# Optimization experiments

Hardware: AMD Instinct MI355X
Metric: run time of the kernel (lower is better)

Reference implementation:

```python
import jax, jax.numpy as jnp
import numpy as np

B, C, H, W = 8, 256, 32, 32
Nh, DK, DV = 8, 64, 64


def conv1x1(x, Wm, b):
    # x: [B,C,H,W], Wm: [O,C] -> [B,O,H,W]
    return jnp.einsum('bchw,oc->bohw', x, Wm) + b[None, :, None, None]


def rel_to_abs(x):
    # x: [B', Nh', L, 2L-1] -> [B', Nh', L, L]
    b, nh, L, _ = x.shape
    x = jnp.pad(x, ((0, 0), (0, 0), (0, 0), (0, 1)))          # [b,nh,L,2L]
    flat = x.reshape(b, nh, L * 2 * L)
    flat = jnp.pad(flat, ((0, 0), (0, 0), (0, L - 1)))
    final = flat.reshape(b, nh, L + 1, 2 * L - 1)
    return final[:, :, :L, L - 1:]


def relative_logits_1d(q, rel_k, Hd, Wd, case):
    # q: [B,Nh,Hd,Wd,dk], rel_k: [2*Wd-1, dk]
    rel = jnp.einsum('bhxyd,md->bhxym', q, rel_k)             # [B,Nh,Hd,Wd,2Wd-1]
    rel = rel.reshape(-1, Nh * Hd, Wd, 2 * Wd - 1)
    rel = rel_to_abs(rel)                                      # [B,Nh*Hd,Wd,Wd]
    rel = rel.reshape(-1, Nh, Hd, Wd, Wd)
    rel = jnp.broadcast_to(rel[:, :, :, None],
                           (rel.shape[0], Nh, Hd, Hd, Wd, Wd))
    if case == 'w':
        rel = rel.transpose((0, 1, 2, 4, 3, 5))                # [B,Nh,H,W,H,W]
    else:  # 'h'
        rel = rel.transpose((0, 1, 4, 2, 5, 3))                # [B,Nh,H,W,H,W]
    return rel.reshape(-1, Nh, Hd * Wd, Hd * Wd)


def setup_inputs() -> dict:
    key = jax.random.key(0)
    ks = jax.random.split(key, 13)
    s = 0.05
    return {
        'q_x': jax.random.normal(ks[0], (B, C, H, W), jnp.float32),
        'k_x': jax.random.normal(ks[1], (B, C, H, W), jnp.float32),
        'v_x': jax.random.normal(ks[2], (B, C, H, W), jnp.float32),
        'Wq': jax.random.normal(ks[3], (Nh * DK, C), jnp.float32) * s,
        'bq': jax.random.normal(ks[4], (Nh * DK,), jnp.float32) * s,
        'Wk': jax.random.normal(ks[5], (Nh * DK, C), jnp.float32) * s,
        'bk': jax.random.normal(ks[6], (Nh * DK,), jnp.float32) * s,
        'Wv': jax.random.normal(ks[7], (Nh * DV, C), jnp.float32) * s,
        'bv': jax.random.normal(ks[8], (Nh * DV,), jnp.float32) * s,
        'Wo': jax.random.normal(ks[9], (DV, Nh * DV), jnp.float32) * s,
        'bo': jax.random.normal(ks[10], (DV,), jnp.float32) * s,
        'key_rel_w': jax.random.normal(ks[11], (2 * W - 1, DK), jnp.float32),
        'key_rel_h': jax.random.normal(ks[12], (2 * H - 1, DK), jnp.float32),
    }


def reference(q_x, k_x, v_x, Wq, bq, Wk, bk, Wv, bv, Wo, bo, key_rel_w, key_rel_h):
    q = conv1x1(q_x, Wq, bq).reshape(B, Nh, DK, H, W) * (DK ** -0.5)
    k = conv1x1(k_x, Wk, bk).reshape(B, Nh, DK, H, W)
    v = conv1x1(v_x, Wv, bv).reshape(B, Nh, DV, H, W)
    flat_q = q.reshape(B, Nh, DK, H * W)
    flat_k = k.reshape(B, Nh, DK, H * W)
    flat_v = v.reshape(B, Nh, DV, H * W)
    # content logits: [B,Nh,HW,HW]
    logits = jnp.einsum('bhdi,bhdj->bhij', flat_q, flat_k)
    # relative logits (Bello et al.)
    qt = q.transpose((0, 1, 3, 4, 2))                          # [B,Nh,H,W,dk]
    w_rel = relative_logits_1d(qt, key_rel_w, H, W, 'w')
    h_rel = relative_logits_1d(qt.transpose((0, 1, 3, 2, 4)), key_rel_h, W, H, 'h')
    logits = logits + h_rel + w_rel
    weights = jax.nn.softmax(logits, axis=-1)
    # [B,Nh,HW,dv] then reshape (NOT transpose) exactly as the torch code does
    attn = jnp.einsum('bhij,bhdj->bhid', weights, flat_v)
    attn = attn.reshape(B, Nh, DV, H, W)
    attn = attn.reshape(B, Nh * DV, H, W)                      # combine heads
    return conv1x1(attn, Wo, bo)                               # [B,dv,H,W]
```

## Files before the change

kernel.cpp:

```cpp
#include <hip/hip_runtime.h>

using f32x4  = __attribute__((ext_vector_type(4))) float;
using f32x16 = __attribute__((ext_vector_type(16))) float;
using bf16x8 = __attribute__((ext_vector_type(8))) short;

__device__ __forceinline__ ushort f2bf(float f) {
  union { float f; unsigned u; } v{f};
  unsigned r = v.u + 0x7FFFu + ((v.u >> 16) & 1u);
  return (ushort)(r >> 16);
}
__device__ __forceinline__ ushort4 f4bf(float4 f) {
  ushort4 r; r.x = f2bf(f.x); r.y = f2bf(f.y); r.z = f2bf(f.z); r.w = f2bf(f.w); return r;
}
__device__ __forceinline__ f32x4 mfma16(bf16x8 a, bf16x8 b, f32x4 c) {
  return __builtin_amdgcn_mfma_f32_16x16x32_bf16(a, b, c, 0, 0, 0);
}
__device__ __forceinline__ f32x16 mfma32(bf16x8 a, bf16x8 b, f32x16 c) {
  return __builtin_amdgcn_mfma_f32_32x32x16_bf16(a, b, c, 0, 0, 0);
}
__device__ __forceinline__ void gload16(const ushort* g, ushort* l) {
  __builtin_amdgcn_global_load_lds(
      (const __attribute__((address_space(1))) void*)g,
      (__attribute__((address_space(3))) void*)l, 16, 0, 0);
}

__global__ __launch_bounds__(256) void prep_all(
    const float* __restrict__ x0, const float* __restrict__ x1,
    const float* __restrict__ x2,
    const float* __restrict__ Wq, const float* __restrict__ Wk,
    const float* __restrict__ Wv, const float* __restrict__ Wo,
    ushort* __restrict__ xT, ushort* __restrict__ Wdst)
{
  __shared__ ushort sT[64 * 72];
  const int bi = blockIdx.x;
  const int t = threadIdx.x;
  if (bi < 1536) {
    const int hw0 = (bi & 15) * 64;
    const int rest = bi >> 4;
    const int y = rest % 12, b = rest / 12;
    const int inp = y >> 2, c0 = (y & 3) * 64;
    const float* src = (inp == 0 ? x0 : inp == 1 ? x1 : x2) +
                       ((size_t)b * 256 + c0) * 1024 + hw0;
    const int clb = t >> 4, hwl = (t & 15) * 4;
#pragma unroll
    for (int cc = 0; cc < 4; ++cc) {
      const int cl = clb + cc * 16;
      const float4 v = *reinterpret_cast<const float4*>(&src[(size_t)cl * 1024 + hwl]);
      *reinterpret_cast<ushort4*>(&sT[cl * 72 + hwl]) = f4bf(v);
    }
    __syncthreads();
    const int hv = t >> 2, cs = (t & 3) * 16;
    ushort tmp[16];
#pragma unroll
    for (int j = 0; j < 16; ++j) tmp[j] = sT[(cs + j) * 72 + hv];
    ushort* dst = xT + (size_t)inp * 2097152 +
                  ((size_t)b * 1024 + hw0 + hv) * 256 + c0 + cs;
    *reinterpret_cast<uint4*>(&dst[0]) = *reinterpret_cast<uint4*>(&tmp[0]);
    *reinterpret_cast<uint4*>(&dst[8]) = *reinterpret_cast<uint4*>(&tmp[8]);
  } else {
    const int idx = ((bi - 1536) * 256 + t) * 8;
    const int r = idx >> 17;
    const float* src = (r == 0 ? Wq : r == 1 ? Wk : r == 2 ? Wv : Wo) + (idx - r * 131072);
    const float4 a = *reinterpret_cast<const float4*>(&src[0]);
    const float4 b = *reinterpret_cast<const float4*>(&src[4]);
    ushort tmp[8];
    *reinterpret_cast<ushort4*>(&tmp[0]) = f4bf(a);
    *reinterpret_cast<ushort4*>(&tmp[4]) = f4bf(b);
    *reinterpret_cast<uint4*>(&Wdst[idx]) = *reinterpret_cast<uint4*>(&tmp[0]);
  }
}

__global__ __launch_bounds__(256) void conv_qkv(
    const ushort* __restrict__ xT, const ushort* __restrict__ WsBf,
    const float* __restrict__ bq, const float* __restrict__ bk,
    const float* __restrict__ bv,
    ushort* __restrict__ outQ, ushort* __restrict__ outK,
    ushort* __restrict__ outV)
{
  __shared__ ushort lds[18432];
  const int z = blockIdx.z, inp = z >> 3, b = z & 7;
  const int t = threadIdx.x, w = t >> 6, lane = t & 63;
  const int li = lane & 15, g = lane >> 4;
  const int o0 = blockIdx.y * 256, hw0 = blockIdx.x * 64;
  const ushort* xb = xT + (size_t)inp * 2097152 + ((size_t)b * 1024 + hw0) * 256;
  const ushort* wb = WsBf + (size_t)inp * 131072 + (size_t)o0 * 256;
  const float* bias = (inp == 0 ? bq : inp == 1 ? bk : bv);
  ushort* out = (inp == 0 ? outQ : inp == 1 ? outK : outV);
  const float scale = (inp == 0) ? 0.125f * 1.44269504f : 1.0f;
  const int MODE = (inp == 2);
  const int srow = t >> 2, sseg = t & 3;

  f32x4 acc[4][4];
#pragma unroll
  for (int i = 0; i < 4; ++i)
#pragma unroll
    for (int j = 0; j < 4; ++j) acc[i][j] = f32x4{0.f, 0.f, 0.f, 0.f};

  for (int ks = 0; ks < 8; ++ks) {
    const int k0 = ks * 32;
    __syncthreads();
    *reinterpret_cast<uint4*>(&lds[srow * 40 + sseg * 8]) =
        *reinterpret_cast<const uint4*>(&xb[(size_t)srow * 256 + k0 + sseg * 8]);
#pragma unroll
    for (int it = 0; it < 4; ++it) {
      const int r = srow + it * 64;
      *reinterpret_cast<uint4*>(&lds[(64 + r) * 40 + sseg * 8]) =
          *reinterpret_cast<const uint4*>(&wb[(size_t)r * 256 + k0 + sseg * 8]);
    }
    __syncthreads();
    bf16x8 af[4], bf[4];
#pragma unroll
    for (int mi = 0; mi < 4; ++mi) {
      const int ra = (!MODE) ? (mi * 16 + li) : (64 + w * 64 + mi * 16 + li);
      af[mi] = *reinterpret_cast<const bf16x8*>(&lds[ra * 40 + g * 8]);
    }
#pragma unroll
    for (int ni = 0; ni < 4; ++ni) {
      const int rb = (!MODE) ? (64 + w * 64 + ni * 16 + li) : (ni * 16 + li);
      bf[ni] = *reinterpret_cast<const bf16x8*>(&lds[rb * 40 + g * 8]);
    }
#pragma unroll
    for (int mi = 0; mi < 4; ++mi)
#pragma unroll
      for (int ni = 0; ni < 4; ++ni)
        acc[mi][ni] = mfma16(af[mi], bf[ni], acc[mi][ni]);
  }
  __syncthreads();

  if (!MODE) {
    float bb[4];
#pragma unroll
    for (int ni = 0; ni < 4; ++ni) bb[ni] = bias[o0 + w * 64 + ni * 16 + li];
#pragma unroll
    for (int mi = 0; mi < 4; ++mi)
#pragma unroll
      for (int ni = 0; ni < 4; ++ni)
#pragma unroll
        for (int r = 0; r < 4; ++r)
          lds[(mi * 16 + g * 4 + r) * 264 + w * 64 + ni * 16 + li] =
              f2bf((acc[mi][ni][r] + bb[ni]) * scale);
    __syncthreads();
    const int row = t & 63;
    ushort* dst = out + (size_t)(b * 8 + (o0 >> 6) + w) * 65536 +
                  (size_t)(hw0 + row) * 64;
#pragma unroll
    for (int seg = 0; seg < 8; ++seg)
      *reinterpret_cast<uint4*>(&dst[seg * 8]) =
          *reinterpret_cast<const uint4*>(&lds[row * 264 + w * 64 + seg * 8]);
  } else {
    const int lis = (li & 3) | ((li & 4) << 1) | ((li & 8) >> 1);
#pragma unroll
    for (int mi = 0; mi < 4; ++mi)
#pragma unroll
      for (int r = 0; r < 4; ++r) {
        const float bb = bias[o0 + w * 64 + mi * 16 + g * 4 + r];
#pragma unroll
        for (int ni = 0; ni < 4; ++ni)
          lds[w * 4608 + (mi * 16 + g * 4 + r) * 72 + ni * 16 + lis] =
              f2bf(acc[mi][ni][r] + bb);
      }
    __syncthreads();
    const int d = t & 63;
    ushort* dst = out + (size_t)(b * 8 + (o0 >> 6) + w) * 65536 +
                  (size_t)d * 1024 + hw0;
#pragma unroll
    for (int seg = 0; seg < 8; ++seg)
      *reinterpret_cast<uint4*>(&dst[seg * 8]) =
          *reinterpret_cast<const uint4*>(&lds[w * 4608 + d * 72 + seg * 8]);
  }
}

__global__ __launch_bounds__(256) void outconv_mfma(
    const float* __restrict__ attnF, const ushort* __restrict__ Wob,
    const float* __restrict__ bias, float* __restrict__ out)
{
  __shared__ float ldsf[64 * 68];
  ushort* lds = reinterpret_cast<ushort*>(ldsf);
  const int t = threadIdx.x, w = t >> 6, lane = t & 63;
  const int li = lane & 15, g = lane >> 4;
  const int b = blockIdx.y, hw0 = blockIdx.x * 64;
  f32x4 acc[4];
#pragma unroll
  for (int i = 0; i < 4; ++i) acc[i] = f32x4{0.f, 0.f, 0.f, 0.f};

  for (int ks = 0; ks < 16; ++ks) {
    const int k0 = ks * 32;
    __syncthreads();
    *reinterpret_cast<uint4*>(&lds[(t >> 2) * 40 + (t & 3) * 8]) =
        *reinterpret_cast<const uint4*>(&Wob[(size_t)(t >> 2) * 512 + k0 + (t & 3) * 8]);
#pragma unroll
    for (int it = 0; it < 2; ++it) {
      const int c = (t >> 4) + it * 16;
      const float4 v = *reinterpret_cast<const float4*>(
          &attnF[((size_t)b * 512 + k0 + c) * 1024 + hw0 + (t & 15) * 4]);
      const int swz = c ^ ((t & 3) << 3);
      const float vv[4] = {v.x, v.y, v.z, v.w};
#pragma unroll
      for (int j = 0; j < 4; ++j)
        lds[2560 + ((t & 15) * 4 + j) * 40 + swz] = f2bf(vv[j]);
    }
    __syncthreads();
    const bf16x8 bfg = *reinterpret_cast<const bf16x8*>(
        &lds[2560 + (w * 16 + li) * 40 + 8 * (g ^ ((li >> 2) & 3))]);
#pragma unroll
    for (int mi = 0; mi < 4; ++mi) {
      const bf16x8 af = *reinterpret_cast<const bf16x8*>(&lds[(mi * 16 + li) * 40 + g * 8]);
      acc[mi] = mfma16(af, bfg, acc[mi]);
    }
  }
  __syncthreads();
#pragma unroll
  for (int mi = 0; mi < 4; ++mi)
#pragma unroll
    for (int r = 0; r < 4; ++r)
      ldsf[(mi * 16 + g * 4 + r) * 68 + w * 16 + li] =
          acc[mi][r] + bias[mi * 16 + g * 4 + r];
  __syncthreads();
  const int o = t >> 2, cs = (t & 3) * 16;
  float* dst = out + ((size_t)b * 64 + o) * 1024 + hw0;
#pragma unroll
  for (int f = 0; f < 4; ++f)
    *reinterpret_cast<float4*>(&dst[cs + f * 4]) =
        *reinterpret_cast<const float4*>(&ldsf[o * 68 + cs + f * 4]);
}

__global__ __launch_bounds__(256, 3) void attn_mfma(
    const ushort* __restrict__ qg, const ushort* __restrict__ kg,
    const ushort* __restrict__ vg, const float* __restrict__ relw,
    const float* __restrict__ relh, float* __restrict__ attn)
{
  __shared__ __align__(16) unsigned char smem[50176];
  ushort* kv0 = (ushort*)smem;
  ushort* kv1 = (ushort*)(smem + 16384);
  float*  scratch = (float*)(smem + 16384);
  float*  rhc = (float*)(smem + 32768);

  const int bid = blockIdx.x;
  const int bn = bid & 63;
  const int qb = (bid >> 6) * 128;
  const int tid = threadIdx.x;
  const int w = tid >> 6, lane = tid & 63;
  const int li32 = lane & 31, h = lane >> 5;
  const int so = lane & 7;

  const ushort* qbn = qg + (size_t)bn * 65536;
  const ushort* kbn = kg + (size_t)bn * 65536;
  const ushort* vbn = vg + (size_t)bn * 65536;

  const int ldr = lane >> 3;
  auto stage = [&](int cc) {
    ushort* dst = (cc & 1) ? kv1 : kv0;
    if (w < 2) {
#pragma unroll
      for (int inst = 0; inst < 4; ++inst) {
        const int row = w * 32 + inst * 8 + ldr;
        const int col8 = ((lane & 7) ^ (row & 7)) * 8;
        gload16(&kbn[(cc * 64 + row) * 64 + col8],
                &dst[(w * 32 + inst * 8) * 64]);
      }
    } else {
#pragma unroll
      for (int inst = 0; inst < 4; ++inst) {
        const int dv = (w - 2) * 32 + inst * 8 + ldr;
        const int col8 = ((lane & 7) ^ (dv & 7)) * 8;
        gload16(&vbn[dv * 1024 + cc * 64 + col8],
                &dst[4096 + ((w - 2) * 32 + inst * 8) * 64]);
      }
    }
  };

  stage(0);

  const int qi = qb + w * 32 + li32;
  bf16x8 qf[4];
#pragma unroll
  for (int ks = 0; ks < 4; ++ks)
    qf[ks] = *reinterpret_cast<const bf16x8*>(&qbn[qi * 64 + ks * 16 + 8 * h]);

  const int xq = (qb + w * 32) >> 5;

  float* tbw = scratch + (size_t)(w * 32) * 66;
  float rwv[16];
#pragma unroll
  for (int mt = 0; mt < 2; ++mt) {
    f32x16 d;
#pragma unroll
    for (int e = 0; e < 16; ++e) d[e] = 0.f;
    const int mm = min(mt * 32 + li32, 62);
#pragma unroll
    for (int ks = 0; ks < 4; ++ks) {
      float tmp[8];
      *reinterpret_cast<float4*>(&tmp[0]) =
          *reinterpret_cast<const float4*>(&relw[mm * 64 + ks * 16 + 8 * h]);
      *reinterpret_cast<float4*>(&tmp[4]) =
          *reinterpret_cast<const float4*>(&relw[mm * 64 + ks * 16 + 8 * h + 4]);
      bf16x8 af;
#pragma unroll
      for (int e = 0; e < 8; ++e) af[e] = (short)f2bf(tmp[e]);
      d = mfma32(af, qf[ks], d);
    }
#pragma unroll
    for (int r = 0; r < 16; ++r)
      tbw[li32 * 66 + mt * 32 + ((r & 3) + 8 * (r >> 2) + 4 * h)] = d[r];
  }
  asm volatile("s_waitcnt lgkmcnt(0)" ::: "memory");
  __builtin_amdgcn_sched_barrier(0);
#pragma unroll
  for (int r = 0; r < 16; ++r)
    rwv[r] = tbw[li32 * 65 + ((r & 3) + 8 * (r >> 2) + 4 * h) + 31];
  asm volatile("s_waitcnt lgkmcnt(0)" ::: "memory");
  __builtin_amdgcn_sched_barrier(0);
  __syncthreads();

#pragma unroll
  for (int mt = 0; mt < 2; ++mt) {
    f32x16 d;
#pragma unroll
    for (int e = 0; e < 16; ++e) d[e] = 0.f;
    const int mm = min(mt * 32 + li32, 62);
#pragma unroll
    for (int ks = 0; ks < 4; ++ks) {
      float tmp[8];
      *reinterpret_cast<float4*>(&tmp[0]) =
          *reinterpret_cast<const float4*>(&relh[mm * 64 + ks * 16 + 8 * h]);
      *reinterpret_cast<float4*>(&tmp[4]) =
          *reinterpret_cast<const float4*>(&relh[mm * 64 + ks * 16 + 8 * h + 4]);
      bf16x8 af;
#pragma unroll
      for (int e = 0; e < 8; ++e) af[e] = (short)f2bf(tmp[e]);
      d = mfma32(af, qf[ks], d);
    }
#pragma unroll
    for (int r = 0; r < 16; ++r) {
      const int m = mt * 32 + ((r & 3) + 8 * (r >> 2) + 4 * h);
      const int idx = m - 31 + xq;
      if ((unsigned)idx < 32u)
        rhc[(w * 32 + li32) * 34 + idx] = d[r];
    }
  }
  asm volatile("s_waitcnt lgkmcnt(0)" ::: "memory");
  __builtin_amdgcn_sched_barrier(0);

  f32x16 oacc0, oacc1;
#pragma unroll
  for (int e = 0; e < 16; ++e) { oacc0[e] = 0.f; oacc1[e] = 0.f; }
  float lrun = 0.f;

  for (int c = 0; c < 16; ++c) {
    __syncthreads();
    if (c < 15) stage(c + 1);
    const ushort* Kb = (c & 1) ? kv1 : kv0;
    const ushort* Vb = Kb + 4096;

    const float2 rhv = *reinterpret_cast<const float2*>(
        &rhc[(w * 32 + li32) * 34 + 2 * c]);
    f32x16 s0, s1;
#pragma unroll
    for (int r = 0; r < 16; ++r) { s0[r] = rwv[r] + rhv.x; s1[r] = rwv[r] + rhv.y; }
    __builtin_amdgcn_s_setprio(1);
#pragma unroll
    for (int ks = 0; ks < 4; ++ks) {
      const int oct = ((2 * ks + h) ^ so) * 8;
      const bf16x8 k0 = *reinterpret_cast<const bf16x8*>(&Kb[li32 * 64 + oct]);
      const bf16x8 k1 = *reinterpret_cast<const bf16x8*>(&Kb[(32 + li32) * 64 + oct]);
      s0 = mfma32(k0, qf[ks], s0);
      s1 = mfma32(k1, qf[ks], s1);
    }
    __builtin_amdgcn_s_setprio(0);

    float psum = 0.f;
#pragma unroll
    for (int r = 0; r < 16; ++r) {
      s0[r] = exp2f(s0[r]);
      s1[r] = exp2f(s1[r]);
      psum += s0[r] + s1[r];
    }
    lrun += psum;

    uint pk0[4][2], pk1[4][2];
#pragma unroll
    for (int J = 0; J < 4; ++J) {
      asm("v_cvt_pk_bf16_f32 %0, %1, %2" : "=v"(pk0[J][0]) : "v"(s0[4 * J]), "v"(s0[4 * J + 1]));
      asm("v_cvt_pk_bf16_f32 %0, %1, %2" : "=v"(pk0[J][1]) : "v"(s0[4 * J + 2]), "v"(s0[4 * J + 3]));
      asm("v_cvt_pk_bf16_f32 %0, %1, %2" : "=v"(pk1[J][0]) : "v"(s1[4 * J]), "v"(s1[4 * J + 1]));
      asm("v_cvt_pk_bf16_f32 %0, %1, %2" : "=v"(pk1[J][1]) : "v"(s1[4 * J + 2]), "v"(s1[4 * J + 3]));
    }

    __builtin_amdgcn_s_setprio(1);
#pragma unroll
    for (int ks = 0; ks < 4; ++ks) {
      const int kk = ks & 1;
      uint fu[4];
      if (ks < 2) {
        fu[0] = pk0[2 * kk][0]; fu[1] = pk0[2 * kk][1];
        fu[2] = pk0[2 * kk + 1][0]; fu[3] = pk0[2 * kk + 1][1];
      } else {
        fu[0] = pk1[2 * kk][0]; fu[1] = pk1[2 * kk][1];
        fu[2] = pk1[2 * kk + 1][0]; fu[3] = pk1[2 * kk + 1][1];
      }
      const bf16x8 pa = *reinterpret_cast<const bf16x8*>(&fu[0]);
      const int oct = ((2 * ks + h) ^ so) * 8;
      const bf16x8 v0 = *reinterpret_cast<const bf16x8*>(&Vb[li32 * 64 + oct]);
      const bf16x8 v1 = *reinterpret_cast<const bf16x8*>(&Vb[(32 + li32) * 64 + oct]);
      oacc0 = mfma32(pa, v0, oacc0);
      oacc1 = mfma32(pa, v1, oacc1);
    }
    __builtin_amdgcn_s_setprio(0);
  }

  const float lt = lrun + __shfl_xor(lrun, 32);
  float* ob = attn + (size_t)bn * 65536;
#pragma unroll
  for (int r = 0; r < 16; ++r) {
    const int rp = (r & 3) + 8 * (r >> 2) + 4 * h;
    const float linv = 1.0f / __shfl(lt, rp);
    const size_t qrow = (size_t)(qb + w * 32 + rp) * 64;
    ob[qrow + li32] = oacc0[r] * linv;
    ob[qrow + 32 + li32] = oacc1[r] * linv;
  }
}

extern "C" void kernel_launch(void* const* d_in, const int* in_sizes, int n_in,
                              void* d_out, int out_size, void* d_ws, size_t ws_size,
                              hipStream_t stream) {
  const float* q_x = (const float*)d_in[0];
  const float* k_x = (const float*)d_in[1];
  const float* v_x = (const float*)d_in[2];
  const float* Wq  = (const float*)d_in[3];
  const float* bq  = (const float*)d_in[4];
  const float* Wk  = (const float*)d_in[5];
  const float* bk  = (const float*)d_in[6];
  const float* Wv  = (const float*)d_in[7];
  const float* bv  = (const float*)d_in[8];
  const float* Wo  = (const float*)d_in[9];
  const float* bo  = (const float*)d_in[10];
  const float* krw = (const float*)d_in[11];
  const float* krh = (const float*)d_in[12];

  ushort* wsQ  = (ushort*)d_ws;
  ushort* wsK  = wsQ + 4194304;
  ushort* wsV  = wsK + 4194304;
  ushort* xT   = wsV + 4194304;
  ushort* WsBf = xT + 6291456;
  float*  attnF = (float*)(WsBf + 425984);

  prep_all<<<1744, 256, 0, stream>>>(q_x, k_x, v_x, Wq, Wk, Wv, Wo, xT, WsBf);

  conv_qkv<<<dim3(16, 2, 24), 256, 0, stream>>>(xT, WsBf, bq, bk, bv, wsQ, wsK, wsV);

  attn_mfma<<<512, 256, 0, stream>>>(wsQ, wsK, wsV, krw, krh, attnF);

  outconv_mfma<<<dim3(16, 8), 256, 0, stream>>>(attnF, WsBf + 393216, bo, (float*)d_out);
}
```

Measured before the change: 90.08 us.

## Halve outconv tile to double block count, use raw exp2 and split sum chains

```diff
diff --git a/kernel.cpp b/kernel.cpp
--- a/kernel.cpp
+++ b/kernel.cpp
@@ -170,15 +170,15 @@
   }
 }
 
-__global__ __launch_bounds__(256) void outconv_mfma(
+__global__ __launch_bounds__(128) void outconv_mfma(
     const float* __restrict__ attnF, const ushort* __restrict__ Wob,
     const float* __restrict__ bias, float* __restrict__ out)
 {
-  __shared__ float ldsf[64 * 68];
-  ushort* lds = reinterpret_cast<ushort*>(ldsf);
-  const int t = threadIdx.x, w = t >> 6, lane = t & 63;
+  __shared__ float ldsf[64 * 36];
+  __shared__ ushort lds[64 * 40 + 32 * 40];
+  const int t = threadIdx.x, wv = t >> 6, lane = t & 63;
   const int li = lane & 15, g = lane >> 4;
-  const int b = blockIdx.y, hw0 = blockIdx.x * 64;
+  const int b = blockIdx.y, hw0 = blockIdx.x * 32;
   f32x4 acc[4];
 #pragma unroll
   for (int i = 0; i < 4; ++i) acc[i] = f32x4{0.f, 0.f, 0.f, 0.f};
@@ -186,22 +186,29 @@
   for (int ks = 0; ks < 16; ++ks) {
     const int k0 = ks * 32;
     __syncthreads();
-    *reinterpret_cast<uint4*>(&lds[(t >> 2) * 40 + (t & 3) * 8]) =
-        *reinterpret_cast<const uint4*>(&Wob[(size_t)(t >> 2) * 512 + k0 + (t & 3) * 8]);
-#pragma unroll
-    for (int it = 0; it < 2; ++it) {
-      const int c = (t >> 4) + it * 16;
-      const float4 v = *reinterpret_cast<const float4*>(
-          &attnF[((size_t)b * 512 + k0 + c) * 1024 + hw0 + (t & 15) * 4]);
-      const int swz = c ^ ((t & 3) << 3);
-      const float vv[4] = {v.x, v.y, v.z, v.w};
-#pragma unroll
-      for (int j = 0; j < 4; ++j)
-        lds[2560 + ((t & 15) * 4 + j) * 40 + swz] = f2bf(vv[j]);
+    {
+      const int row = t & 63, sh = (t >> 6) * 16;
+      *reinterpret_cast<uint4*>(&lds[row * 40 + sh]) =
+          *reinterpret_cast<const uint4*>(&Wob[(size_t)row * 512 + k0 + sh]);
+      *reinterpret_cast<uint4*>(&lds[row * 40 + sh + 8]) =
+          *reinterpret_cast<const uint4*>(&Wob[(size_t)row * 512 + k0 + sh + 8]);
+    }
+    {
+      const int c = t >> 2, hw8 = (t & 3) * 8;
+      const float* src = &attnF[((size_t)b * 512 + k0 + c) * 1024 + hw0 + hw8];
+      const float4 a4 = *reinterpret_cast<const float4*>(&src[0]);
+      const float4 b4 = *reinterpret_cast<const float4*>(&src[4]);
+      const float vv[8] = {a4.x, a4.y, a4.z, a4.w, b4.x, b4.y, b4.z, b4.w};
+#pragma unroll
+      for (int e = 0; e < 8; ++e) {
+        const int hw = hw8 + e;
+        const int swz = c ^ (((hw >> 2) & 3) << 3);
+        lds[2560 + hw * 40 + swz] = f2bf(vv[e]);
+      }
     }
     __syncthreads();
     const bf16x8 bfg = *reinterpret_cast<const bf16x8*>(
-        &lds[2560 + (w * 16 + li) * 40 + 8 * (g ^ ((li >> 2) & 3))]);
+        &lds[2560 + (wv * 16 + li) * 40 + 8 * (g ^ ((li >> 2) & 3))]);
 #pragma unroll
     for (int mi = 0; mi < 4; ++mi) {
       const bf16x8 af = *reinterpret_cast<const bf16x8*>(&lds[(mi * 16 + li) * 40 + g * 8]);
@@ -213,15 +220,15 @@
   for (int mi = 0; mi < 4; ++mi)
 #pragma unroll
     for (int r = 0; r < 4; ++r)
-      ldsf[(mi * 16 + g * 4 + r) * 68 + w * 16 + li] =
+      ldsf[(mi * 16 + g * 4 + r) * 36 + wv * 16 + li] =
           acc[mi][r] + bias[mi * 16 + g * 4 + r];
   __syncthreads();
-  const int o = t >> 2, cs = (t & 3) * 16;
-  float* dst = out + ((size_t)b * 64 + o) * 1024 + hw0;
+  const int o = t >> 1, half = (t & 1) * 16;
+  float* dst = out + ((size_t)b * 64 + o) * 1024 + hw0 + half;
 #pragma unroll
   for (int f = 0; f < 4; ++f)
-    *reinterpret_cast<float4*>(&dst[cs + f * 4]) =
-        *reinterpret_cast<const float4*>(&ldsf[o * 68 + cs + f * 4]);
+    *reinterpret_cast<float4*>(&dst[f * 4]) =
+        *reinterpret_cast<const float4*>(&ldsf[o * 36 + half + f * 4]);
 }
 
 __global__ __launch_bounds__(256, 3) void attn_mfma(
@@ -368,14 +375,22 @@
     }
     __builtin_amdgcn_s_setprio(0);
 
-    float psum = 0.f;
 #pragma unroll
     for (int r = 0; r < 16; ++r) {
-      s0[r] = exp2f(s0[r]);
-      s1[r] = exp2f(s1[r]);
-      psum += s0[r] + s1[r];
-    }
-    lrun += psum;
+      s0[r] = __builtin_amdgcn_exp2f(s0[r]);
+      s1[r] = __builtin_amdgcn_exp2f(s1[r]);
+    }
+    {
+      float q0 = 0.f, q1 = 0.f, q2 = 0.f, q3 = 0.f;
+#pragma unroll
+      for (int r = 0; r < 16; r += 4) {
+        q0 += s0[r + 0] + s1[r + 0];
+        q1 += s0[r + 1] + s1[r + 1];
+        q2 += s0[r + 2] + s1[r + 2];
+        q3 += s0[r + 3] + s1[r + 3];
+      }
+      lrun += (q0 + q1) + (q2 + q3);
+    }
 
     uint pk0[4][2], pk1[4][2];
 #pragma unroll
@@ -450,5 +465,5 @@
 
   attn_mfma<<<512, 256, 0, stream>>>(wsQ, wsK, wsV, krw, krh, attnF);
 
-  outconv_mfma<<<dim3(16, 8), 256, 0, stream>>>(attnF, WsBf + 393216, bo, (float*)d_out);
-}
+  outconv_mfma<<<dim3(32, 8), 128, 0, stream>>>(attnF, WsBf + 393216, bo, (float*)d_out);
+}
```

New measurement: 81.83 us. -9.2%, faster.
